# Kernel optimization log

Measured on AMD Instinct MI355X. Metric: run time of the kernel, lower is better.

The kernel has to match this reference:

```python
import jax, jax.numpy as jnp
import numpy as np

STRIDE = 8


def setup_inputs() -> dict:
    key = jax.random.key(0)
    ks = jax.random.split(key, 4)
    C, K = 256, 32  # in_chn, key_channel = in_chn // 8
    B, H, W = 4, 256, 256
    return {
        "features": jax.random.normal(ks[0], (B, C, H, W), dtype=jnp.float32),
        "q_w": jax.random.normal(ks[1], (K, C), dtype=jnp.float32) * 0.05,
        "q_b": jnp.zeros((K,), dtype=jnp.float32),
        "k_w": jax.random.normal(ks[2], (K, C), dtype=jnp.float32) * 0.05,
        "k_b": jnp.zeros((K,), dtype=jnp.float32),
        "v_w": jax.random.normal(ks[3], (C, C), dtype=jnp.float32) * 0.05,
        "v_b": jnp.zeros((C,), dtype=jnp.float32),
    }


def reference(features, q_w, q_b, k_w, k_b, v_w, v_b):
    B, C, H, W = features.shape
    s = STRIDE
    Hp, Wp = H // s, W // s
    N = Hp * Wp
    K = q_w.shape[0]

    # AvgPool2d(stride): non-overlapping s x s mean
    x = features.reshape(B, C, Hp, s, Wp, s).mean(axis=(3, 5))  # [B,C,Hp,Wp]
    xf = x.reshape(B, C, N)  # flatten spatial tokens

    # 1x1 convs == channel contractions
    q = jnp.einsum('kc,bcn->bkn', q_w, xf) + q_b[None, :, None]  # [B,K,N]
    k = jnp.einsum('kc,bcn->bkn', k_w, xf) + k_b[None, :, None]  # [B,K,N]
    v = jnp.einsum('oc,bcn->bon', v_w, xf) + v_b[None, :, None]  # [B,C,N]

    # energy[b,n,m] = sum_k q[b,k,n] * k[b,k,m], scaled by key_channel**-0.5
    scale = jnp.asarray(K, features.dtype) ** -0.5
    energy = jnp.einsum('bkn,bkm->bnm', q, k) * scale  # [B,N,N]
    attention = jax.nn.softmax(energy, axis=-1)

    # out[b,c,n] = sum_m v[b,c,m] * attention[b,n,m]
    out = jnp.einsum('bcm,bnm->bcn', v, attention).reshape(B, C, Hp, Wp)

    # F.interpolate(..., [Hp*s, Wp*s]) default nearest -> exact sxs repeat
    out = jnp.repeat(jnp.repeat(out, s, axis=2), s, axis=3)  # [B,C,H,W]
    return out + features
```

## Files before the change

kernel.cpp:

```cpp
#include <hip/hip_runtime.h>
#include <hip/hip_bf16.h>

#define B_ 4
#define C_ 256
#define H_ 256
#define W_ 256
#define N_ 1024
#define KC 32

typedef __attribute__((ext_vector_type(8))) short short8;
typedef __attribute__((ext_vector_type(4))) float floatx4;

__device__ __forceinline__ short f2bf(float x) {
    __hip_bfloat16 h = __float2bfloat16(x);
    return *reinterpret_cast<const short*>(&h);
}

__global__ void pool_kernel(const float* __restrict__ feat, short* __restrict__ xfT) {
    const int hp = blockIdx.x;
    const int cc = blockIdx.y;
    const int b  = blockIdx.z;
    const int t  = threadIdx.x;
    const int ci = t >> 5, wp = t & 31;
    const int c = cc * 8 + ci;
    const float* base = feat + (((size_t)(b * C_ + c) * H_ + hp * 8) * W_) + wp * 8;
    float s = 0.f;
#pragma unroll
    for (int r = 0; r < 8; ++r) {
        const float4* p = reinterpret_cast<const float4*>(base + (size_t)r * W_);
        float4 a = p[0], d = p[1];
        s += a.x + a.y + a.z + a.w + d.x + d.y + d.z + d.w;
    }
    s *= (1.f / 64.f);
    __shared__ float lds[32][9];
    lds[wp][ci] = s;
    __syncthreads();
    if (t < 32) {
        short8 v;
#pragma unroll
        for (int j = 0; j < 8; ++j) v[j] = f2bf(lds[t][j]);
        *reinterpret_cast<short8*>(xfT + ((size_t)(b * N_ + hp * 32 + t) * C_) + cc * 8) = v;
    }
}

__global__ void qkv_kernel(const short* __restrict__ xfT,
                           const float* __restrict__ q_w, const float* __restrict__ q_b,
                           const float* __restrict__ k_w, const float* __restrict__ k_b,
                           const float* __restrict__ v_w, const float* __restrict__ v_b,
                           short* __restrict__ qkT, short* __restrict__ vmat) {
    const int b = blockIdx.y;
    const int t = threadIdx.x, wv = t >> 6, l = t & 63;
    const int lr = l & 15, lg = l >> 4;
    if (blockIdx.x < 16) {
        const int nblk = blockIdx.x;
        const int nbase = nblk * 64 + wv * 16;
        floatx4 acc[4] = {};
        for (int ks = 0; ks < 8; ++ks) {
            const int cb = ks * 32 + lg * 8;
            short8 afrag = *reinterpret_cast<const short8*>(
                xfT + ((size_t)(b * N_ + nbase + lr) * C_) + cb);
#pragma unroll
            for (int ot = 0; ot < 4; ++ot) {
                const int o = ot * 16 + lr;
                const float* wrow = (o < 32) ? (q_w + (size_t)o * C_) : (k_w + (size_t)(o - 32) * C_);
                const float4* wp4 = reinterpret_cast<const float4*>(wrow + cb);
                float4 w0 = wp4[0], w1 = wp4[1];
                short8 bfrag;
                bfrag[0] = f2bf(w0.x); bfrag[1] = f2bf(w0.y); bfrag[2] = f2bf(w0.z); bfrag[3] = f2bf(w0.w);
                bfrag[4] = f2bf(w1.x); bfrag[5] = f2bf(w1.y); bfrag[6] = f2bf(w1.z); bfrag[7] = f2bf(w1.w);
                acc[ot] = __builtin_amdgcn_mfma_f32_16x16x32_bf16(afrag, bfrag, acc[ot], 0, 0, 0);
            }
        }
#pragma unroll
        for (int ot = 0; ot < 4; ++ot) {
            const int o = ot * 16 + lr;
            const float bias = (o < 32) ? q_b[o] : k_b[o - 32];
#pragma unroll
            for (int r = 0; r < 4; ++r) {
                const int n = nbase + lg * 4 + r;
                qkT[((size_t)(b * N_ + n)) * 64 + o] = f2bf(acc[ot][r] + bias);
            }
        }
    } else {
        const int idx = blockIdx.x - 16;
        const int nblk = idx & 15, cblk = idx >> 4;
        const int cbase = cblk * 64 + wv * 16;
        const int nbase = nblk * 64;
        floatx4 acc[4] = {};
        for (int ks = 0; ks < 8; ++ks) {
            const int cin = ks * 32 + lg * 8;
            const float4* wp4 = reinterpret_cast<const float4*>(v_w + (size_t)(cbase + lr) * C_ + cin);
            float4 w0 = wp4[0], w1 = wp4[1];
            short8 afrag;
            afrag[0] = f2bf(w0.x); afrag[1] = f2bf(w0.y); afrag[2] = f2bf(w0.z); afrag[3] = f2bf(w0.w);
            afrag[4] = f2bf(w1.x); afrag[5] = f2bf(w1.y); afrag[6] = f2bf(w1.z); afrag[7] = f2bf(w1.w);
#pragma unroll
            for (int nt = 0; nt < 4; ++nt) {
                short8 bfrag = *reinterpret_cast<const short8*>(
                    xfT + ((size_t)(b * N_ + nbase + nt * 16 + lr)) * C_ + cin);
                acc[nt] = __builtin_amdgcn_mfma_f32_16x16x32_bf16(afrag, bfrag, acc[nt], 0, 0, 0);
            }
        }
#pragma unroll
        for (int nt = 0; nt < 4; ++nt) {
#pragma unroll
            for (int r = 0; r < 4; ++r) {
                const int c = cbase + lg * 4 + r;
                const int n = nbase + nt * 16 + lr;
                vmat[((size_t)(b * C_ + c)) * N_ + n] = f2bf(acc[nt][r] + v_b[c]);
            }
        }
    }
}

__global__ void attn_kernel(const short* __restrict__ qkT, short* __restrict__ att) {
    const int nblk = blockIdx.x, b = blockIdx.y;
    const int t = threadIdx.x, wv = t >> 6, l = t & 63;
    const int lr = l & 15, lg = l >> 4;
    const int nbase = nblk * 16;
    short8 afrag = *reinterpret_cast<const short8*>(
        qkT + ((size_t)(b * N_ + nbase + lr)) * 64 + lg * 8);
    floatx4 acc[16] = {};
#pragma unroll
    for (int mt = 0; mt < 16; ++mt) {
        const int m = wv * 256 + mt * 16 + lr;
        short8 bfrag = *reinterpret_cast<const short8*>(
            qkT + ((size_t)(b * N_ + m)) * 64 + 32 + lg * 8);
        acc[mt] = __builtin_amdgcn_mfma_f32_16x16x32_bf16(afrag, bfrag, acc[mt], 0, 0, 0);
    }
    const float scale = 0.17677669529663688f;
#pragma unroll
    for (int mt = 0; mt < 16; ++mt) acc[mt] *= scale;

    __shared__ float smax[4][16];
    __shared__ float ssum[4][16];
    float mx[4], sm[4];
#pragma unroll
    for (int r = 0; r < 4; ++r) {
        float m = acc[0][r];
#pragma unroll
        for (int mt = 1; mt < 16; ++mt) m = fmaxf(m, acc[mt][r]);
        for (int off = 1; off < 16; off <<= 1) m = fmaxf(m, __shfl_xor(m, off, 64));
        mx[r] = m;
    }
    if (lr == 0) {
#pragma unroll
        for (int r = 0; r < 4; ++r) smax[wv][lg * 4 + r] = mx[r];
    }
    __syncthreads();
#pragma unroll
    for (int r = 0; r < 4; ++r) {
        float m = smax[0][lg * 4 + r];
        for (int w = 1; w < 4; ++w) m = fmaxf(m, smax[w][lg * 4 + r]);
        mx[r] = m;
        sm[r] = 0.f;
    }
#pragma unroll
    for (int mt = 0; mt < 16; ++mt) {
#pragma unroll
        for (int r = 0; r < 4; ++r) {
            float p = __expf(acc[mt][r] - mx[r]);
            acc[mt][r] = p;
            sm[r] += p;
        }
    }
#pragma unroll
    for (int r = 0; r < 4; ++r) {
        float s = sm[r];
        for (int off = 1; off < 16; off <<= 1) s += __shfl_xor(s, off, 64);
        sm[r] = s;
    }
    if (lr == 0) {
#pragma unroll
        for (int r = 0; r < 4; ++r) ssum[wv][lg * 4 + r] = sm[r];
    }
    __syncthreads();
    float inv[4];
#pragma unroll
    for (int r = 0; r < 4; ++r) {
        float s = 0.f;
        for (int w = 0; w < 4; ++w) s += ssum[w][lg * 4 + r];
        inv[r] = 1.f / s;
    }
#pragma unroll
    for (int mt = 0; mt < 16; ++mt) {
#pragma unroll
        for (int r = 0; r < 4; ++r) {
            att[((size_t)(b * N_ + nbase + lg * 4 + r)) * N_ + wv * 256 + mt * 16 + lr] =
                f2bf(acc[mt][r] * inv[r]);
        }
    }
}

__global__ void pv_kernel(const short* __restrict__ att, const short* __restrict__ vmat,
                          float* __restrict__ outsT) {
    const int nblk = blockIdx.x, b = blockIdx.y;
    const int t = threadIdx.x, wv = t >> 6, l = t & 63;
    const int lr = l & 15, lg = l >> 4;
    const int nbase = nblk * 16;
    const int cbase = wv * 32;
    floatx4 acc[2] = {};
    const short* attrow = att + ((size_t)(b * N_ + nbase + lr)) * N_;
    const short* vrow0 = vmat + ((size_t)(b * C_ + cbase + lr)) * N_;
    const short* vrow1 = vmat + ((size_t)(b * C_ + cbase + 16 + lr)) * N_;
#pragma unroll 4
    for (int ks = 0; ks < 32; ++ks) {
        const int mb = ks * 32 + lg * 8;
        short8 afrag = *reinterpret_cast<const short8*>(attrow + mb);
        short8 b0 = *reinterpret_cast<const short8*>(vrow0 + mb);
        short8 b1 = *reinterpret_cast<const short8*>(vrow1 + mb);
        acc[0] = __builtin_amdgcn_mfma_f32_16x16x32_bf16(afrag, b0, acc[0], 0, 0, 0);
        acc[1] = __builtin_amdgcn_mfma_f32_16x16x32_bf16(afrag, b1, acc[1], 0, 0, 0);
    }
#pragma unroll
    for (int ct = 0; ct < 2; ++ct) {
#pragma unroll
        for (int r = 0; r < 4; ++r) {
            outsT[((size_t)(b * N_ + nbase + lg * 4 + r)) * C_ + cbase + ct * 16 + lr] =
                acc[ct][r];
        }
    }
}

__global__ void final_kernel(const float* __restrict__ feat, const float* __restrict__ outsT,
                             float* __restrict__ out) {
    const int t = threadIdx.x;
    const size_t R = (size_t)blockIdx.x * 4 + (t >> 6);
    const int wi = t & 63;
    const int b = (int)(R >> 16);
    const int c = (int)((R >> 8) & 255);
    const int h = (int)(R & 255);
    const int hp = h >> 3, wp = wi >> 1;
    const size_t base = R * 256 + (size_t)wi * 4;
    float4 f = *reinterpret_cast<const float4*>(feat + base);
    const float s = outsT[((size_t)(b * N_ + hp * 32 + wp)) * C_ + c];
    f.x += s; f.y += s; f.z += s; f.w += s;
    *reinterpret_cast<float4*>(out + base) = f;
}

extern "C" void kernel_launch(void* const* d_in, const int* in_sizes, int n_in,
                              void* d_out, int out_size, void* d_ws, size_t ws_size,
                              hipStream_t stream) {
    const float* feat = (const float*)d_in[0];
    const float* q_w  = (const float*)d_in[1];
    const float* q_b  = (const float*)d_in[2];
    const float* k_w  = (const float*)d_in[3];
    const float* k_b  = (const float*)d_in[4];
    const float* v_w  = (const float*)d_in[5];
    const float* v_b  = (const float*)d_in[6];
    float* out = (float*)d_out;

    char* ws = (char*)d_ws;
    short* xfT   = (short*)(ws);
    short* qkT   = (short*)(ws + 2097152);
    short* vmat  = (short*)(ws + 2621440);
    short* att   = (short*)(ws + 4718592);
    float* outsT = (float*)(ws + 13107200);

    pool_kernel <<<dim3(32, 32, B_), 256, 0, stream>>>(feat, xfT);
    qkv_kernel  <<<dim3(80, B_),     256, 0, stream>>>(xfT, q_w, q_b, k_w, k_b, v_w, v_b, qkT, vmat);
    attn_kernel <<<dim3(64, B_),     256, 0, stream>>>(qkT, att);
    pv_kernel   <<<dim3(64, B_),     512, 0, stream>>>(att, vmat, outsT);
    final_kernel<<<65536,            256, 0, stream>>>(feat, outsT, out);
}
```

Measured before the change: 538.4 us.

## Fuse attention softmax and PV matmul into one kernel via LDS

Merges the attention-softmax kernel and the PV matmul kernel into a single 512-thread kernel. The normalized probabilities stay in a swizzled 32KB shared-memory tile and are no longer written to and re-read from an 8MB bf16 global attention buffer. Each block now spreads its 16 query rows across 8 waves of 128 keys each, which saves one launch and the global round trip. The cost is higher LDS use per block and an extra barrier before the PV phase.

```diff
diff --git a/kernel.cpp b/kernel.cpp
--- a/kernel.cpp
+++ b/kernel.cpp
@@ -113,33 +113,37 @@
     }
 }
 
-__global__ void attn_kernel(const short* __restrict__ qkT, short* __restrict__ att) {
+__global__ void attnpv_kernel(const short* __restrict__ qkT, const short* __restrict__ vmat,
+                              float* __restrict__ outsT) {
     const int nblk = blockIdx.x, b = blockIdx.y;
     const int t = threadIdx.x, wv = t >> 6, l = t & 63;
     const int lr = l & 15, lg = l >> 4;
     const int nbase = nblk * 16;
+
+    __shared__ short plds[16 * 1024];
+    __shared__ float smax[8][16];
+    __shared__ float ssum[8][16];
+
     short8 afrag = *reinterpret_cast<const short8*>(
         qkT + ((size_t)(b * N_ + nbase + lr)) * 64 + lg * 8);
-    floatx4 acc[16] = {};
-#pragma unroll
-    for (int mt = 0; mt < 16; ++mt) {
-        const int m = wv * 256 + mt * 16 + lr;
+    floatx4 acc[8] = {};
+#pragma unroll
+    for (int mt = 0; mt < 8; ++mt) {
+        const int m = wv * 128 + mt * 16 + lr;
         short8 bfrag = *reinterpret_cast<const short8*>(
             qkT + ((size_t)(b * N_ + m)) * 64 + 32 + lg * 8);
         acc[mt] = __builtin_amdgcn_mfma_f32_16x16x32_bf16(afrag, bfrag, acc[mt], 0, 0, 0);
     }
     const float scale = 0.17677669529663688f;
 #pragma unroll
-    for (int mt = 0; mt < 16; ++mt) acc[mt] *= scale;
-
-    __shared__ float smax[4][16];
-    __shared__ float ssum[4][16];
+    for (int mt = 0; mt < 8; ++mt) acc[mt] *= scale;
+
     float mx[4], sm[4];
 #pragma unroll
     for (int r = 0; r < 4; ++r) {
         float m = acc[0][r];
 #pragma unroll
-        for (int mt = 1; mt < 16; ++mt) m = fmaxf(m, acc[mt][r]);
+        for (int mt = 1; mt < 8; ++mt) m = fmaxf(m, acc[mt][r]);
         for (int off = 1; off < 16; off <<= 1) m = fmaxf(m, __shfl_xor(m, off, 64));
         mx[r] = m;
     }
@@ -151,12 +155,13 @@
 #pragma unroll
     for (int r = 0; r < 4; ++r) {
         float m = smax[0][lg * 4 + r];
-        for (int w = 1; w < 4; ++w) m = fmaxf(m, smax[w][lg * 4 + r]);
+#pragma unroll
+        for (int w = 1; w < 8; ++w) m = fmaxf(m, smax[w][lg * 4 + r]);
         mx[r] = m;
         sm[r] = 0.f;
     }
 #pragma unroll
-    for (int mt = 0; mt < 16; ++mt) {
+    for (int mt = 0; mt < 8; ++mt) {
 #pragma unroll
         for (int r = 0; r < 4; ++r) {
             float p = __expf(acc[mt][r] - mx[r]);
@@ -179,45 +184,41 @@
 #pragma unroll
     for (int r = 0; r < 4; ++r) {
         float s = 0.f;
-        for (int w = 0; w < 4; ++w) s += ssum[w][lg * 4 + r];
+#pragma unroll
+        for (int w = 0; w < 8; ++w) s += ssum[w][lg * 4 + r];
         inv[r] = 1.f / s;
     }
 #pragma unroll
-    for (int mt = 0; mt < 16; ++mt) {
+    for (int mt = 0; mt < 8; ++mt) {
 #pragma unroll
         for (int r = 0; r < 4; ++r) {
-            att[((size_t)(b * N_ + nbase + lg * 4 + r)) * N_ + wv * 256 + mt * 16 + lr] =
-                f2bf(acc[mt][r] * inv[r]);
-        }
-    }
-}
-
-__global__ void pv_kernel(const short* __restrict__ att, const short* __restrict__ vmat,
-                          float* __restrict__ outsT) {
-    const int nblk = blockIdx.x, b = blockIdx.y;
-    const int t = threadIdx.x, wv = t >> 6, l = t & 63;
-    const int lr = l & 15, lg = l >> 4;
-    const int nbase = nblk * 16;
+            const int row = lg * 4 + r;
+            const int col = wv * 128 + mt * 16 + lr;
+            plds[(row * 1024 + col) ^ ((row & 7) << 3)] = f2bf(acc[mt][r] * inv[r]);
+        }
+    }
+    __syncthreads();
+
     const int cbase = wv * 32;
-    floatx4 acc[2] = {};
-    const short* attrow = att + ((size_t)(b * N_ + nbase + lr)) * N_;
+    floatx4 oacc[2] = {};
     const short* vrow0 = vmat + ((size_t)(b * C_ + cbase + lr)) * N_;
     const short* vrow1 = vmat + ((size_t)(b * C_ + cbase + 16 + lr)) * N_;
 #pragma unroll 4
     for (int ks = 0; ks < 32; ++ks) {
         const int mb = ks * 32 + lg * 8;
-        short8 afrag = *reinterpret_cast<const short8*>(attrow + mb);
+        short8 pa = *reinterpret_cast<const short8*>(
+            &plds[(lr * 1024 + mb) ^ ((lr & 7) << 3)]);
         short8 b0 = *reinterpret_cast<const short8*>(vrow0 + mb);
         short8 b1 = *reinterpret_cast<const short8*>(vrow1 + mb);
-        acc[0] = __builtin_amdgcn_mfma_f32_16x16x32_bf16(afrag, b0, acc[0], 0, 0, 0);
-        acc[1] = __builtin_amdgcn_mfma_f32_16x16x32_bf16(afrag, b1, acc[1], 0, 0, 0);
+        oacc[0] = __builtin_amdgcn_mfma_f32_16x16x32_bf16(pa, b0, oacc[0], 0, 0, 0);
+        oacc[1] = __builtin_amdgcn_mfma_f32_16x16x32_bf16(pa, b1, oacc[1], 0, 0, 0);
     }
 #pragma unroll
     for (int ct = 0; ct < 2; ++ct) {
 #pragma unroll
         for (int r = 0; r < 4; ++r) {
             outsT[((size_t)(b * N_ + nbase + lg * 4 + r)) * C_ + cbase + ct * 16 + lr] =
-                acc[ct][r];
+                oacc[ct][r];
         }
     }
 }
@@ -254,12 +255,10 @@
     short* xfT   = (short*)(ws);
     short* qkT   = (short*)(ws + 2097152);
     short* vmat  = (short*)(ws + 2621440);
-    short* att   = (short*)(ws + 4718592);
-    float* outsT = (float*)(ws + 13107200);
-
-    pool_kernel <<<dim3(32, 32, B_), 256, 0, stream>>>(feat, xfT);
-    qkv_kernel  <<<dim3(80, B_),     256, 0, stream>>>(xfT, q_w, q_b, k_w, k_b, v_w, v_b, qkT, vmat);
-    attn_kernel <<<dim3(64, B_),     256, 0, stream>>>(qkT, att);
-    pv_kernel   <<<dim3(64, B_),     512, 0, stream>>>(att, vmat, outsT);
-    final_kernel<<<65536,            256, 0, stream>>>(feat, outsT, out);
-}
+    float* outsT = (float*)(ws + 4718592);
+
+    pool_kernel  <<<dim3(32, 32, B_), 256, 0, stream>>>(feat, xfT);
+    qkv_kernel   <<<dim3(80, B_),     256, 0, stream>>>(xfT, q_w, q_b, k_w, k_b, v_w, v_b, qkT, vmat);
+    attnpv_kernel<<<dim3(64, B_),     512, 0, stream>>>(qkT, vmat, outsT);
+    final_kernel <<<65536,            256, 0, stream>>>(feat, outsT, out);
+}
```

Result: no change. 529.6 us (-1.6%).
